# Kernel tuning notes

Measured on AMD Instinct MI355X. Metric: run time of the kernel, lower is better.

Reference implementation:

```python
import jax, jax.numpy as jnp
import numpy as np

DIM = 192
HEADS = 16
DIM_HEAD = 64
INNER = HEADS * DIM_HEAD  # 1024
B, N = 8, 1024


def setup_inputs() -> dict:
    key = jax.random.key(0)
    ks = jax.random.split(key, 8)
    x = jax.random.normal(ks[0], (B, N, DIM), dtype=jnp.float32)
    shift = jax.random.normal(ks[1], (B, 1, DIM), dtype=jnp.float32)
    scale = jax.random.normal(ks[2], (B, 1, DIM), dtype=jnp.float32)
    norm_w = jnp.ones((DIM,), dtype=jnp.float32)
    norm_b = jnp.zeros((DIM,), dtype=jnp.float32)
    w_qkv = jax.random.normal(ks[3], (DIM, 3 * INNER), dtype=jnp.float32) * (DIM ** -0.5)
    w_out = jax.random.normal(ks[4], (INNER, DIM), dtype=jnp.float32) * (INNER ** -0.5)
    b_out = jnp.zeros((DIM,), dtype=jnp.float32)
    return {"x": x, "shift": shift, "scale": scale, "norm_w": norm_w,
            "norm_b": norm_b, "w_qkv": w_qkv, "w_out": w_out, "b_out": b_out}


def _layernorm(x, w, b, eps=1e-5):
    mu = jnp.mean(x, axis=-1, keepdims=True)
    var = jnp.mean(jnp.square(x - mu), axis=-1, keepdims=True)
    return (x - mu) * jax.lax.rsqrt(var + eps) * w + b


def reference(x, shift, scale, norm_w, norm_b, w_qkv, w_out, b_out):
    h = _layernorm(x, norm_w, norm_b)
    h = h * (1.0 + scale) + shift  # adaLN modulation, broadcast over tokens
    qkv = h @ w_qkv  # [B, N, 3*INNER]
    q, k, v = jnp.split(qkv, 3, axis=-1)
    # [B, N, INNER] -> [B, H, N, Dh]
    def split_heads(t):
        return t.reshape(B, N, HEADS, DIM_HEAD).transpose(0, 2, 1, 3)
    q, k, v = split_heads(q), split_heads(k), split_heads(v)
    scores = jnp.einsum('bhnd,bhmd->bhnm', q, k) * (DIM_HEAD ** -0.5)
    attn = jax.nn.softmax(scores, axis=-1)
    out = jnp.einsum('bhnm,bhmd->bhnd', attn, v)  # [B, H, N, Dh]
    out = out.transpose(0, 2, 1, 3).reshape(B, N, INNER)
    return out @ w_out + b_out
```

## Files before the change

### kernel.cpp

```cpp
#include <hip/hip_runtime.h>

#define DIM 192
#define NB 8
#define NTOK 1024
#define HEADS 16
#define DH 64
#define INNER 1024
#define ROWS (NB * NTOK)

typedef __bf16 bf16x8 __attribute__((ext_vector_type(8)));
typedef float f32x4 __attribute__((ext_vector_type(4)));
typedef float f32x16 __attribute__((ext_vector_type(16)));
typedef unsigned int u32x4 __attribute__((ext_vector_type(4)));

__device__ inline unsigned short f2bf(float f) {
    union { float f; unsigned u; } v; v.f = f;
    unsigned r = v.u + 0x7FFF + ((v.u >> 16) & 1);
    return (unsigned short)(r >> 16);
}

__device__ inline unsigned pk2(float a, float b) {
    __bf16 x = (__bf16)a, y = (__bf16)b;
    unsigned short ux = __builtin_bit_cast(unsigned short, x);
    unsigned short uy = __builtin_bit_cast(unsigned short, y);
    return (unsigned)ux | ((unsigned)uy << 16);
}

__device__ inline void gl_lds16(const unsigned short* g, unsigned short* l) {
    __builtin_amdgcn_global_load_lds(
        (const __attribute__((address_space(1))) void*)g,
        (__attribute__((address_space(3))) void*)l, 16, 0, 0);
}

__device__ inline size_t fragIdx(int row, int k, int depth) {
    return ((size_t)(row >> 5) * ((size_t)depth * 4) +
            (size_t)(((k >> 4) * 2 + ((k >> 3) & 1)) * 32 + (row & 31))) * 8 + (k & 7);
}

__global__ __launch_bounds__(256) void k_pre(
    const float* __restrict__ x, const float* __restrict__ shift,
    const float* __restrict__ scale, const float* __restrict__ nw,
    const float* __restrict__ nb, const float* __restrict__ wqkv,
    const float* __restrict__ wout,
    unsigned short* __restrict__ hF, unsigned short* __restrict__ wF,
    unsigned short* __restrict__ woF) {
    int bid = blockIdx.x;
    if (bid < 2048) {
        int row = bid * 4 + (threadIdx.x >> 6);
        int lane = threadIdx.x & 63;
        const float* xr = x + row * DIM;
        float v0 = xr[lane], v1 = xr[lane + 64], v2 = xr[lane + 128];
        float s = v0 + v1 + v2;
        #pragma unroll
        for (int m = 1; m < 64; m <<= 1) s += __shfl_xor(s, m);
        float mean = s * (1.0f / DIM);
        float d0 = v0 - mean, d1 = v1 - mean, d2 = v2 - mean;
        float q = d0 * d0 + d1 * d1 + d2 * d2;
        #pragma unroll
        for (int m = 1; m < 64; m <<= 1) q += __shfl_xor(q, m);
        float rs = rsqrtf(q * (1.0f / DIM) + 1e-5f);
        int b = row >> 10;
        float vv[3] = {v0, v1, v2};
        #pragma unroll
        for (int i = 0; i < 3; i++) {
            int d = lane + 64 * i;
            float val = (vv[i] - mean) * rs * nw[d] + nb[d];
            val = val * (1.0f + scale[b * DIM + d]) + shift[b * DIM + d];
            hF[fragIdx(row, d, DIM)] = f2bf(val);
        }
    } else if (bid < 4352) {
        int idx = (bid - 2048) * 256 + threadIdx.x;
        int k = idx / 3072, c = idx % 3072;
        wF[fragIdx(c, k, DIM)] = f2bf(wqkv[idx]);
    } else {
        int idx = (bid - 4352) * 256 + threadIdx.x;
        int k = idx / 192, c = idx % 192;
        woF[fragIdx(c, k, INNER)] = f2bf(wout[idx]);
    }
}

__global__ __launch_bounds__(256, 3) void k_qkv(
    const unsigned short* __restrict__ hF, const unsigned short* __restrict__ wF,
    unsigned short* __restrict__ qm, unsigned short* __restrict__ km,
    unsigned short* __restrict__ vtm) {
    const float QSC = 0.125f * 1.4426950408889634f;
    int tid = threadIdx.x;
    int wave = tid >> 6, lane = tid & 63;
    int l31 = lane & 31, hi = lane >> 5;
    int c0 = blockIdx.x * 64 + (wave >> 1) * 32;
    int typ = c0 >> 10;
    int hd  = (c0 & 1023) >> 6;
    int coff = c0 & 32;

    const unsigned short* Ab = wF + (size_t)(c0 >> 5) * 768 * 8;
    bf16x8 af[12];
    #pragma unroll
    for (int kc = 0; kc < 12; kc++)
        af[kc] = *(const bf16x8*)(Ab + ((kc * 2 + hi) * 32 + l31) * 8);

    #pragma unroll
    for (int ns = 0; ns < 2; ns++) {
        int n0 = blockIdx.y * 128 + (wave & 1) * 64 + ns * 32;
        const unsigned short* Bb = hF + (size_t)(n0 >> 5) * 768 * 8;
        f32x16 acc;
        #pragma unroll
        for (int r = 0; r < 16; r++) acc[r] = 0.f;
        #pragma unroll
        for (int kc = 0; kc < 12; kc++) {
            bf16x8 bf = *(const bf16x8*)(Bb + ((kc * 2 + hi) * 32 + l31) * 8);
            acc = __builtin_amdgcn_mfma_f32_32x32x16_bf16(af[kc], bf, acc, 0, 0, 0);
        }
        int n = n0 + l31, bb = n >> 10, nm = n & 1023;
        if (typ < 2) {
            float sc = (typ == 0) ? QSC : 1.0f;
            unsigned short* base = (typ == 0 ? qm : km) +
                ((size_t)(bb * 16 + hd) * 1024 + nm) * 64;
            #pragma unroll
            for (int rg = 0; rg < 4; rg++) {
                uint2 val;
                val.x = pk2(acc[rg * 4 + 0] * sc, acc[rg * 4 + 1] * sc);
                val.y = pk2(acc[rg * 4 + 2] * sc, acc[rg * 4 + 3] * sc);
                *(uint2*)(base + coff + rg * 8 + hi * 4) = val;
            }
        } else {
            unsigned short* base = vtm + (size_t)(bb * 16 + hd) * 65536 + nm;
            #pragma unroll
            for (int r = 0; r < 16; r++) {
                int d = coff + (r & 3) + 8 * (r >> 2) + 4 * hi;
                base[(size_t)d * 1024] = f2bf(acc[r]);
            }
        }
    }
}

__global__ __launch_bounds__(256, 4) void k_attn(
    const unsigned short* __restrict__ qm, const unsigned short* __restrict__ km,
    const unsigned short* __restrict__ vtm, unsigned short* __restrict__ attnF) {
    __shared__ __align__(128) unsigned short Kb[2][4096];
    __shared__ __align__(128) unsigned short Vb[3][4096];

    int tid = threadIdx.x;
    int wave = tid >> 6, lane = tid & 63;
    int l31 = lane & 31, hi = lane >> 5;
    int bh = blockIdx.x, qt = blockIdx.y;
    int qbase = qt * 128 + wave * 32;
    const unsigned short* Q = qm + (size_t)bh * NTOK * DH;
    const unsigned short* K = km + (size_t)bh * NTOK * DH;
    const unsigned short* VT = vtm + (size_t)bh * DH * NTOK;

    bf16x8 qf[4];
    #pragma unroll
    for (int c = 0; c < 4; c++)
        qf[c] = *(const bf16x8*)(Q + (qbase + l31) * DH + c * 16 + hi * 8);

    u32x4 ov; ov[0] = 0x3F803F80u; ov[1] = 0x3F803F80u; ov[2] = 0x3F803F80u; ov[3] = 0x3F803F80u;
    bf16x8 ones = __builtin_bit_cast(bf16x8, ov);

    f32x16 accO[2], accL;
    #pragma unroll
    for (int r = 0; r < 16; r++) { accO[0][r] = 0.f; accO[1][r] = 0.f; accL[r] = 0.f; }

    auto stageK = [&](int b, int t) {
        #pragma unroll
        for (int r = 0; r < 2; r++) {
            int off = (tid + r * 256) * 16;
            int row = off >> 7, col = off & 127;
            int scol = col ^ ((row & 7) << 4);
            gl_lds16(K + (t * 64 + row) * DH + (scol >> 1),
                     (unsigned short*)((char*)Kb[b] + off));
        }
    };
    auto stageV = [&](int b, int t) {
        #pragma unroll
        for (int r = 0; r < 2; r++) {
            int off = (tid + r * 256) * 16;
            int row = off >> 7, col = off & 127;
            int scol = col ^ ((row & 7) << 4);
            gl_lds16(VT + (size_t)row * NTOK + t * 64 + (scol >> 1),
                     (unsigned short*)((char*)Vb[b] + off));
        }
    };
    auto ldK = [&](int b, int row, int col) -> bf16x8 {
        int scol = col ^ ((row & 7) << 4);
        return *(const bf16x8*)((const char*)Kb[b] + row * 128 + scol);
    };
    auto ldV = [&](int b, int row, int col) -> bf16x8 {
        int scol = col ^ ((row & 7) << 4);
        return *(const bf16x8*)((const char*)Vb[b] + row * 128 + scol);
    };
    auto packP = [&](const f32x16& P, bf16x8& w0, bf16x8& w1) {
        u32x4 A, B;
        {
            auto r0 = __builtin_amdgcn_permlane32_swap(pk2(P[0], P[1]), pk2(P[4], P[5]), false, false);
            auto r1 = __builtin_amdgcn_permlane32_swap(pk2(P[2], P[3]), pk2(P[6], P[7]), false, false);
            A[0] = r0[0]; A[1] = r1[0]; A[2] = r0[1]; A[3] = r1[1];
        }
        {
            auto r0 = __builtin_amdgcn_permlane32_swap(pk2(P[8], P[9]), pk2(P[12], P[13]), false, false);
            auto r1 = __builtin_amdgcn_permlane32_swap(pk2(P[10], P[11]), pk2(P[14], P[15]), false, false);
            B[0] = r0[0]; B[1] = r1[0]; B[2] = r0[1]; B[3] = r1[1];
        }
        w0 = __builtin_bit_cast(bf16x8, A);
        w1 = __builtin_bit_cast(bf16x8, B);
    };

    bf16x8 pw[4];

    stageK(0, 0); stageV(0, 0);
    __syncthreads();

    stageK(1, 1); stageV(1, 1);
    {
        f32x16 C0, C1;
        #pragma unroll
        for (int r = 0; r < 16; r++) { C0[r] = 0.f; C1[r] = 0.f; }
        __builtin_amdgcn_s_setprio(1);
        #pragma unroll
        for (int c = 0; c < 4; c++) {
            bf16x8 kf = ldK(0, l31, c * 32 + hi * 16);
            C0 = __builtin_amdgcn_mfma_f32_32x32x16_bf16(kf, qf[c], C0, 0, 0, 0);
            bf16x8 kf2 = ldK(0, 32 + l31, c * 32 + hi * 16);
            C1 = __builtin_amdgcn_mfma_f32_32x32x16_bf16(kf2, qf[c], C1, 0, 0, 0);
        }
        __builtin_amdgcn_s_setprio(0);
        #pragma unroll
        for (int r = 0; r < 16; r++) {
            C0[r] = __builtin_amdgcn_exp2f(C0[r]);
            C1[r] = __builtin_amdgcn_exp2f(C1[r]);
        }
        packP(C0, pw[0], pw[1]);
        packP(C1, pw[2], pw[3]);
        #pragma unroll
        for (int kcc = 0; kcc < 4; kcc++)
            accL = __builtin_amdgcn_mfma_f32_32x32x16_bf16(ones, pw[kcc], accL, 0, 0, 0);
        __syncthreads();
    }

    for (int t = 1; t < 16; t++) {
        int kc = t & 1;
        int vp = (t - 1) % 3;
        if (t < 15) { stageK((t + 1) & 1, t + 1); stageV((t + 1) % 3, t + 1); }

        f32x16 C0, C1;
        #pragma unroll
        for (int r = 0; r < 16; r++) { C0[r] = 0.f; C1[r] = 0.f; }
        __builtin_amdgcn_s_setprio(1);
        #pragma unroll
        for (int c = 0; c < 4; c++) {
            bf16x8 kf = ldK(kc, l31, c * 32 + hi * 16);
            C0 = __builtin_amdgcn_mfma_f32_32x32x16_bf16(kf, qf[c], C0, 0, 0, 0);
            bf16x8 kf2 = ldK(kc, 32 + l31, c * 32 + hi * 16);
            C1 = __builtin_amdgcn_mfma_f32_32x32x16_bf16(kf2, qf[c], C1, 0, 0, 0);
        }
        #pragma unroll
        for (int dt = 0; dt < 2; dt++) {
            #pragma unroll
            for (int kcc = 0; kcc < 4; kcc++) {
                bf16x8 vf = ldV(vp, dt * 32 + l31, kcc * 32 + hi * 16);
                accO[dt] = __builtin_amdgcn_mfma_f32_32x32x16_bf16(vf, pw[kcc], accO[dt], 0, 0, 0);
            }
        }
        __builtin_amdgcn_s_setprio(0);

        #pragma unroll
        for (int r = 0; r < 16; r++) {
            C0[r] = __builtin_amdgcn_exp2f(C0[r]);
            C1[r] = __builtin_amdgcn_exp2f(C1[r]);
        }
        packP(C0, pw[0], pw[1]);
        packP(C1, pw[2], pw[3]);
        #pragma unroll
        for (int kcc = 0; kcc < 4; kcc++)
            accL = __builtin_amdgcn_mfma_f32_32x32x16_bf16(ones, pw[kcc], accL, 0, 0, 0);
        __syncthreads();
    }

    __builtin_amdgcn_s_setprio(1);
    #pragma unroll
    for (int dt = 0; dt < 2; dt++) {
        #pragma unroll
        for (int kcc = 0; kcc < 4; kcc++) {
            bf16x8 vf = ldV(0, dt * 32 + l31, kcc * 32 + hi * 16);
            accO[dt] = __builtin_amdgcn_mfma_f32_32x32x16_bf16(vf, pw[kcc], accO[dt], 0, 0, 0);
        }
    }
    __builtin_amdgcn_s_setprio(0);

    float inv = 1.0f / accL[0];
    int b = bh >> 4, hd = bh & 15;
    int rowblk = b * 32 + qt * 4 + wave;
    #pragma unroll
    for (int dt = 0; dt < 2; dt++)
        #pragma unroll
        for (int rq = 0; rq < 4; rq++) {
            int g = (hd * 4 + dt * 2 + (rq >> 1)) * 2 + (rq & 1);
            uint2 val;
            val.x = pk2(accO[dt][rq * 4 + 0] * inv, accO[dt][rq * 4 + 1] * inv);
            val.y = pk2(accO[dt][rq * 4 + 2] * inv, accO[dt][rq * 4 + 3] * inv);
            *(uint2*)((char*)attnF + ((size_t)rowblk * 4096 + g * 32 + l31) * 16 + hi * 8) = val;
        }
}

__global__ __launch_bounds__(256, 2) void k_out(
    const unsigned short* __restrict__ attnF, const unsigned short* __restrict__ woF,
    const float* __restrict__ bias, float* __restrict__ out) {
    int wave = threadIdx.x >> 6, lane = threadIdx.x & 63;
    int l31 = lane & 31, hi = lane >> 5;
    int W = blockIdx.x * 4 + wave;
    int nb = W / 6, cb = W % 6;
    const unsigned short* A = attnF + (size_t)nb * 4096 * 8;
    const unsigned short* B = woF + (size_t)cb * 4096 * 8;

    f32x16 acc;
    #pragma unroll
    for (int r = 0; r < 16; r++) acc[r] = 0.f;
    #pragma unroll 16
    for (int kc = 0; kc < 64; kc++) {
        bf16x8 a = *(const bf16x8*)(A + ((kc * 2 + hi) * 32 + l31) * 8);
        bf16x8 b = *(const bf16x8*)(B + ((kc * 2 + hi) * 32 + l31) * 8);
        acc = __builtin_amdgcn_mfma_f32_32x32x16_bf16(a, b, acc, 0, 0, 0);
    }
    float bi = bias[cb * 32 + l31];
    #pragma unroll
    for (int r = 0; r < 16; r++) {
        int n = nb * 32 + (r & 3) + 8 * (r >> 2) + 4 * hi;
        out[(size_t)n * DIM + cb * 32 + l31] = acc[r] + bi;
    }
}

extern "C" void kernel_launch(void* const* d_in, const int* in_sizes, int n_in,
                              void* d_out, int out_size, void* d_ws, size_t ws_size,
                              hipStream_t stream) {
    const float* x     = (const float*)d_in[0];
    const float* shift = (const float*)d_in[1];
    const float* scale = (const float*)d_in[2];
    const float* nw    = (const float*)d_in[3];
    const float* nbv   = (const float*)d_in[4];
    const float* wqkv  = (const float*)d_in[5];
    const float* wout  = (const float*)d_in[6];
    const float* bout  = (const float*)d_in[7];
    float* out = (float*)d_out;

    char* ws = (char*)d_ws;
    unsigned short* hF    = (unsigned short*)(ws + 0);
    unsigned short* wF    = (unsigned short*)(ws + 3145728);
    unsigned short* woF   = (unsigned short*)(ws + 3145728 + 1179648);
    unsigned short* qm    = (unsigned short*)(ws + 4718592);
    unsigned short* km    = (unsigned short*)(ws + 4718592 + 16777216);
    unsigned short* vtm   = (unsigned short*)(ws + 4718592 + 2 * 16777216);
    unsigned short* attnF = (unsigned short*)(ws + 4718592 + 3 * 16777216);

    k_pre<<<dim3(5120), dim3(256), 0, stream>>>(x, shift, scale, nw, nbv, wqkv, wout, hF, wF, woF);
    k_qkv<<<dim3(48, 64), dim3(256), 0, stream>>>(hF, wF, qm, km, vtm);
    k_attn<<<dim3(128, 8), dim3(256), 0, stream>>>(qm, km, vtm, attnF);
    k_out<<<dim3(384), dim3(256), 0, stream>>>(attnF, woF, bout, out);
}
```

Measured before the change: 102.6 us.

## Give each attention wave two query tiles and sum softmax denominators on VALU

The attention kernel now runs 2 waves per block, each handling 64 query rows as two 32-row tiles. Each K and V fragment read from LDS is reused for two MFMAs, halving LDS reads per MFMA. The row-sum denominator is no longer computed with a ones-vector MFMA. It is accumulated with scalar VALU adds plus a cross-half shuffle, which removes four MFMAs per tile. The cost is roughly double the accumulator registers per wave and fewer waves per block, which may lower occupancy and latency hiding.

```diff
diff --git a/kernel.cpp b/kernel.cpp
--- a/kernel.cpp
+++ b/kernel.cpp
@@ -133,7 +133,7 @@
     }
 }
 
-__global__ __launch_bounds__(256, 4) void k_attn(
+__global__ __launch_bounds__(128, 2) void k_attn(
     const unsigned short* __restrict__ qm, const unsigned short* __restrict__ km,
     const unsigned short* __restrict__ vtm, unsigned short* __restrict__ attnF) {
     __shared__ __align__(128) unsigned short Kb[2][4096];
@@ -143,27 +143,30 @@
     int wave = tid >> 6, lane = tid & 63;
     int l31 = lane & 31, hi = lane >> 5;
     int bh = blockIdx.x, qt = blockIdx.y;
-    int qbase = qt * 128 + wave * 32;
+    int qbase = qt * 128 + wave * 64;
     const unsigned short* Q = qm + (size_t)bh * NTOK * DH;
     const unsigned short* K = km + (size_t)bh * NTOK * DH;
     const unsigned short* VT = vtm + (size_t)bh * DH * NTOK;
 
-    bf16x8 qf[4];
-    #pragma unroll
-    for (int c = 0; c < 4; c++)
-        qf[c] = *(const bf16x8*)(Q + (qbase + l31) * DH + c * 16 + hi * 8);
-
-    u32x4 ov; ov[0] = 0x3F803F80u; ov[1] = 0x3F803F80u; ov[2] = 0x3F803F80u; ov[3] = 0x3F803F80u;
-    bf16x8 ones = __builtin_bit_cast(bf16x8, ov);
-
-    f32x16 accO[2], accL;
-    #pragma unroll
-    for (int r = 0; r < 16; r++) { accO[0][r] = 0.f; accO[1][r] = 0.f; accL[r] = 0.f; }
+    bf16x8 qfA[4], qfB[4];
+    #pragma unroll
+    for (int c = 0; c < 4; c++) {
+        qfA[c] = *(const bf16x8*)(Q + (qbase + l31) * DH + c * 16 + hi * 8);
+        qfB[c] = *(const bf16x8*)(Q + (qbase + 32 + l31) * DH + c * 16 + hi * 8);
+    }
+
+    float lA = 0.f, lB = 0.f;
+    f32x16 accOA[2], accOB[2];
+    #pragma unroll
+    for (int r = 0; r < 16; r++) {
+        accOA[0][r] = 0.f; accOA[1][r] = 0.f;
+        accOB[0][r] = 0.f; accOB[1][r] = 0.f;
+    }
 
     auto stageK = [&](int b, int t) {
         #pragma unroll
-        for (int r = 0; r < 2; r++) {
-            int off = (tid + r * 256) * 16;
+        for (int r = 0; r < 4; r++) {
+            int off = (tid + r * 128) * 16;
             int row = off >> 7, col = off & 127;
             int scol = col ^ ((row & 7) << 4);
             gl_lds16(K + (t * 64 + row) * DH + (scol >> 1),
@@ -172,8 +175,8 @@
     };
     auto stageV = [&](int b, int t) {
         #pragma unroll
-        for (int r = 0; r < 2; r++) {
-            int off = (tid + r * 256) * 16;
+        for (int r = 0; r < 4; r++) {
+            int off = (tid + r * 128) * 16;
             int row = off >> 7, col = off & 127;
             int scol = col ^ ((row & 7) << 4);
             gl_lds16(VT + (size_t)row * NTOK + t * 64 + (scol >> 1),
@@ -203,36 +206,48 @@
         w0 = __builtin_bit_cast(bf16x8, A);
         w1 = __builtin_bit_cast(bf16x8, B);
     };
-
-    bf16x8 pw[4];
+    auto tsum = [](const f32x16& P) -> float {
+        float s0 = (P[0] + P[1]) + (P[2] + P[3]);
+        float s1 = (P[4] + P[5]) + (P[6] + P[7]);
+        float s2 = (P[8] + P[9]) + (P[10] + P[11]);
+        float s3 = (P[12] + P[13]) + (P[14] + P[15]);
+        return (s0 + s1) + (s2 + s3);
+    };
+
+    bf16x8 pwA[4], pwB[4];
 
     stageK(0, 0); stageV(0, 0);
     __syncthreads();
 
     stageK(1, 1); stageV(1, 1);
     {
-        f32x16 C0, C1;
-        #pragma unroll
-        for (int r = 0; r < 16; r++) { C0[r] = 0.f; C1[r] = 0.f; }
+        f32x16 C0A, C0B, C1A, C1B;
+        #pragma unroll
+        for (int r = 0; r < 16; r++) { C0A[r] = 0.f; C0B[r] = 0.f; C1A[r] = 0.f; C1B[r] = 0.f; }
         __builtin_amdgcn_s_setprio(1);
         #pragma unroll
         for (int c = 0; c < 4; c++) {
             bf16x8 kf = ldK(0, l31, c * 32 + hi * 16);
-            C0 = __builtin_amdgcn_mfma_f32_32x32x16_bf16(kf, qf[c], C0, 0, 0, 0);
+            C0A = __builtin_amdgcn_mfma_f32_32x32x16_bf16(kf, qfA[c], C0A, 0, 0, 0);
+            C0B = __builtin_amdgcn_mfma_f32_32x32x16_bf16(kf, qfB[c], C0B, 0, 0, 0);
             bf16x8 kf2 = ldK(0, 32 + l31, c * 32 + hi * 16);
-            C1 = __builtin_amdgcn_mfma_f32_32x32x16_bf16(kf2, qf[c], C1, 0, 0, 0);
+            C1A = __builtin_amdgcn_mfma_f32_32x32x16_bf16(kf2, qfA[c], C1A, 0, 0, 0);
+            C1B = __builtin_amdgcn_mfma_f32_32x32x16_bf16(kf2, qfB[c], C1B, 0, 0, 0);
         }
         __builtin_amdgcn_s_setprio(0);
         #pragma unroll
         for (int r = 0; r < 16; r++) {
-            C0[r] = __builtin_amdgcn_exp2f(C0[r]);
-            C1[r] = __builtin_amdgcn_exp2f(C1[r]);
-        }
-        packP(C0, pw[0], pw[1]);
-        packP(C1, pw[2], pw[3]);
-        #pragma unroll
-        for (int kcc = 0; kcc < 4; kcc++)
-            accL = __builtin_amdgcn_mfma_f32_32x32x16_bf16(ones, pw[kcc], accL, 0, 0, 0);
+            C0A[r] = __builtin_amdgcn_exp2f(C0A[r]);
+            C0B[r] = __builtin_amdgcn_exp2f(C0B[r]);
+            C1A[r] = __builtin_amdgcn_exp2f(C1A[r]);
+            C1B[r] = __builtin_amdgcn_exp2f(C1B[r]);
+        }
+        lA += tsum(C0A) + tsum(C1A);
+        lB += tsum(C0B) + tsum(C1B);
+        packP(C0A, pwA[0], pwA[1]);
+        packP(C1A, pwA[2], pwA[3]);
+        packP(C0B, pwB[0], pwB[1]);
+        packP(C1B, pwB[2], pwB[3]);
         __syncthreads();
     }
 
@@ -241,37 +256,43 @@
         int vp = (t - 1) % 3;
         if (t < 15) { stageK((t + 1) & 1, t + 1); stageV((t + 1) % 3, t + 1); }
 
-        f32x16 C0, C1;
-        #pragma unroll
-        for (int r = 0; r < 16; r++) { C0[r] = 0.f; C1[r] = 0.f; }
+        f32x16 C0A, C0B, C1A, C1B;
+        #pragma unroll
+        for (int r = 0; r < 16; r++) { C0A[r] = 0.f; C0B[r] = 0.f; C1A[r] = 0.f; C1B[r] = 0.f; }
         __builtin_amdgcn_s_setprio(1);
         #pragma unroll
         for (int c = 0; c < 4; c++) {
             bf16x8 kf = ldK(kc, l31, c * 32 + hi * 16);
-            C0 = __builtin_amdgcn_mfma_f32_32x32x16_bf16(kf, qf[c], C0, 0, 0, 0);
+            C0A = __builtin_amdgcn_mfma_f32_32x32x16_bf16(kf, qfA[c], C0A, 0, 0, 0);
+            C0B = __builtin_amdgcn_mfma_f32_32x32x16_bf16(kf, qfB[c], C0B, 0, 0, 0);
             bf16x8 kf2 = ldK(kc, 32 + l31, c * 32 + hi * 16);
-            C1 = __builtin_amdgcn_mfma_f32_32x32x16_bf16(kf2, qf[c], C1, 0, 0, 0);
+            C1A = __builtin_amdgcn_mfma_f32_32x32x16_bf16(kf2, qfA[c], C1A, 0, 0, 0);
+            C1B = __builtin_amdgcn_mfma_f32_32x32x16_bf16(kf2, qfB[c], C1B, 0, 0, 0);
         }
         #pragma unroll
         for (int dt = 0; dt < 2; dt++) {
             #pragma unroll
             for (int kcc = 0; kcc < 4; kcc++) {
                 bf16x8 vf = ldV(vp, dt * 32 + l31, kcc * 32 + hi * 16);
-                accO[dt] = __builtin_amdgcn_mfma_f32_32x32x16_bf16(vf, pw[kcc], accO[dt], 0, 0, 0);
+                accOA[dt] = __builtin_amdgcn_mfma_f32_32x32x16_bf16(vf, pwA[kcc], accOA[dt], 0, 0, 0);
+                accOB[dt] = __builtin_amdgcn_mfma_f32_32x32x16_bf16(vf, pwB[kcc], accOB[dt], 0, 0, 0);
             }
         }
         __builtin_amdgcn_s_setprio(0);
 
         #pragma unroll
         for (int r = 0; r < 16; r++) {
-            C0[r] = __builtin_amdgcn_exp2f(C0[r]);
-            C1[r] = __builtin_amdgcn_exp2f(C1[r]);
-        }
-        packP(C0, pw[0], pw[1]);
-        packP(C1, pw[2], pw[3]);
-        #pragma unroll
-        for (int kcc = 0; kcc < 4; kcc++)
-            accL = __builtin_amdgcn_mfma_f32_32x32x16_bf16(ones, pw[kcc], accL, 0, 0, 0);
+            C0A[r] = __builtin_amdgcn_exp2f(C0A[r]);
+            C0B[r] = __builtin_amdgcn_exp2f(C0B[r]);
+            C1A[r] = __builtin_amdgcn_exp2f(C1A[r]);
+            C1B[r] = __builtin_amdgcn_exp2f(C1B[r]);
+        }
+        lA += tsum(C0A) + tsum(C1A);
+        lB += tsum(C0B) + tsum(C1B);
+        packP(C0A, pwA[0], pwA[1]);
+        packP(C1A, pwA[2], pwA[3]);
+        packP(C0B, pwB[0], pwB[1]);
+        packP(C1B, pwB[2], pwB[3]);
         __syncthreads();
     }
 
@@ -281,24 +302,32 @@
         #pragma unroll
         for (int kcc = 0; kcc < 4; kcc++) {
             bf16x8 vf = ldV(0, dt * 32 + l31, kcc * 32 + hi * 16);
-            accO[dt] = __builtin_amdgcn_mfma_f32_32x32x16_bf16(vf, pw[kcc], accO[dt], 0, 0, 0);
+            accOA[dt] = __builtin_amdgcn_mfma_f32_32x32x16_bf16(vf, pwA[kcc], accOA[dt], 0, 0, 0);
+            accOB[dt] = __builtin_amdgcn_mfma_f32_32x32x16_bf16(vf, pwB[kcc], accOB[dt], 0, 0, 0);
         }
     }
     __builtin_amdgcn_s_setprio(0);
 
-    float inv = 1.0f / accL[0];
+    float invA = 1.0f / (lA + __shfl_xor(lA, 32));
+    float invB = 1.0f / (lB + __shfl_xor(lB, 32));
     int b = bh >> 4, hd = bh & 15;
-    int rowblk = b * 32 + qt * 4 + wave;
-    #pragma unroll
-    for (int dt = 0; dt < 2; dt++)
-        #pragma unroll
-        for (int rq = 0; rq < 4; rq++) {
-            int g = (hd * 4 + dt * 2 + (rq >> 1)) * 2 + (rq & 1);
-            uint2 val;
-            val.x = pk2(accO[dt][rq * 4 + 0] * inv, accO[dt][rq * 4 + 1] * inv);
-            val.y = pk2(accO[dt][rq * 4 + 2] * inv, accO[dt][rq * 4 + 3] * inv);
-            *(uint2*)((char*)attnF + ((size_t)rowblk * 4096 + g * 32 + l31) * 16 + hi * 8) = val;
-        }
+    int rowblkA = b * 32 + qt * 4 + wave * 2;
+    #pragma unroll
+    for (int half = 0; half < 2; half++) {
+        const f32x16* accO = half ? accOB : accOA;
+        float inv = half ? invB : invA;
+        int rowblk = rowblkA + half;
+        #pragma unroll
+        for (int dt = 0; dt < 2; dt++)
+            #pragma unroll
+            for (int rq = 0; rq < 4; rq++) {
+                int g = (hd * 4 + dt * 2 + (rq >> 1)) * 2 + (rq & 1);
+                uint2 val;
+                val.x = pk2(accO[dt][rq * 4 + 0] * inv, accO[dt][rq * 4 + 1] * inv);
+                val.y = pk2(accO[dt][rq * 4 + 2] * inv, accO[dt][rq * 4 + 3] * inv);
+                *(uint2*)((char*)attnF + ((size_t)rowblk * 4096 + g * 32 + l31) * 16 + hi * 8) = val;
+            }
+    }
 }
 
 __global__ __launch_bounds__(256, 2) void k_out(
@@ -352,6 +381,6 @@
 
     k_pre<<<dim3(5120), dim3(256), 0, stream>>>(x, shift, scale, nw, nbv, wqkv, wout, hF, wF, woF);
     k_qkv<<<dim3(48, 64), dim3(256), 0, stream>>>(hF, wF, qm, km, vtm);
-    k_attn<<<dim3(128, 8), dim3(256), 0, stream>>>(qm, km, vtm, attnF);
+    k_attn<<<dim3(128, 8), dim3(128), 0, stream>>>(qm, km, vtm, attnF);
     k_out<<<dim3(384), dim3(256), 0, stream>>>(attnF, woF, bout, out);
 }
```

New measurement: 101.8 us. Within noise of the previous version (-0.8%).
